# Performance work log

Hardware: AMD Instinct MI355X
Metric: run time of the kernel (lower is better)

Reference implementation:

```python
import jax, jax.numpy as jnp
import numpy as np

NUM_HEADS = 16
D_MODEL = 1024
D_K = D_MODEL // NUM_HEADS
B, S = 2, 2048


def setup_inputs() -> dict:
    key = jax.random.key(0)
    ks = jax.random.split(key, 10)
    q = jax.random.normal(ks[0], (B, S, D_MODEL), dtype=jnp.float32)
    k = jax.random.normal(ks[1], (B, S, D_MODEL), dtype=jnp.float32)
    v = jax.random.normal(ks[2], (B, S, D_MODEL), dtype=jnp.float32)
    # causal mask, 1 = keep, 0 = masked (masked_fill(mask==0, -1e9))
    mask = jnp.tril(jnp.ones((S, S), dtype=jnp.int32))[None, None, :, :]
    # Linear weights ~ N(0, 0.02); biases left at torch default-ish small uniform
    std = 0.02
    Wq = jax.random.normal(ks[3], (D_MODEL, D_MODEL), dtype=jnp.float32) * std
    Wk = jax.random.normal(ks[4], (D_MODEL, D_MODEL), dtype=jnp.float32) * std
    Wv = jax.random.normal(ks[5], (D_MODEL, D_MODEL), dtype=jnp.float32) * std
    bound = 1.0 / np.sqrt(D_MODEL)
    bq = jax.random.uniform(ks[6], (D_MODEL,), jnp.float32, -bound, bound)
    bk = jax.random.uniform(ks[7], (D_MODEL,), jnp.float32, -bound, bound)
    bv = jax.random.uniform(ks[8], (D_MODEL,), jnp.float32, -bound, bound)
    return {"q": q, "k": k, "v": v, "mask": mask,
            "Wq": Wq, "bq": bq, "Wk": Wk, "bk": bk, "Wv": Wv, "bv": bv}


def reference(q, k, v, mask, Wq, bq, Wk, bk, Wv, bv):
    # projections (torch Linear: x @ W.T + b), split heads -> [B, H, S, Dk]
    def proj(x, W, b):
        y = x @ W.T + b
        return y.reshape(B, S, NUM_HEADS, D_K).transpose(0, 2, 1, 3)

    qh, kh, vh = proj(q, Wq, bq), proj(k, Wk, bk), proj(v, Wv, bv)
    scores = jnp.einsum('bhqd,bhkd->bhqk', qh, kh) / jnp.sqrt(jnp.float32(D_K))
    scores = jnp.where(mask == 0, jnp.float32(-1e9), scores)
    p = jax.nn.softmax(scores, axis=-1)
    # dropout is identity in eval mode
    x = jnp.einsum('bhqk,bhkd->bhqd', p, vh)  # [B, H, S, Dk]
    return x.transpose(0, 2, 1, 3).reshape(B, S, D_MODEL)
```

## Files before the change

kernel.cpp:

```cpp
#include <hip/hip_runtime.h>

#define B_ 2
#define H_ 16
#define S_ 2048
#define DM 1024
#define DK 64
#define NX (4096 * 1024)

typedef unsigned short u16;
typedef __attribute__((ext_vector_type(8))) short bf16x8;
typedef __attribute__((ext_vector_type(8))) unsigned short u16x8;
typedef __attribute__((ext_vector_type(4))) unsigned short u16x4;
typedef __attribute__((ext_vector_type(2))) unsigned int u32x2;
typedef __attribute__((ext_vector_type(4))) unsigned int u32x4;
typedef __attribute__((ext_vector_type(4))) float f32x4;

__device__ inline u16 f2bf(float f) {
  union { float f; unsigned int u; } c; c.f = f;
  unsigned int u = c.u;
  u += 0x7fffu + ((u >> 16) & 1u);
  return (u16)(u >> 16);
}

__device__ inline void glds16(const u16* g, u16* l) {
  __builtin_amdgcn_global_load_lds(
      (const __attribute__((address_space(1))) unsigned int*)g,
      (__attribute__((address_space(3))) unsigned int*)l, 16, 0, 0);
}

__device__ inline unsigned cvtpk(float lo, float hi) {
  unsigned r;
  asm("v_cvt_pk_bf16_f32 %0, %1, %2" : "=v"(r) : "v"(lo), "v"(hi));
  return r;
}

__device__ inline void pub8(u16* d, float4 a, float4 b) {
  u32x4 r;
  r[0] = cvtpk(a.x, a.y); r[1] = cvtpk(a.z, a.w);
  r[2] = cvtpk(b.x, b.y); r[3] = cvtpk(b.z, b.w);
  *reinterpret_cast<u32x4*>(d) = r;
}

__global__ __launch_bounds__(256) void proj_kernel(
    const float* __restrict__ Xq, const float* __restrict__ Xk, const float* __restrict__ Xv,
    const float* __restrict__ Wq, const float* __restrict__ Wk, const float* __restrict__ Wv,
    const float* __restrict__ bq, const float* __restrict__ bk, const float* __restrict__ bv,
    u16* __restrict__ Qh, u16* __restrict__ Kh, u16* __restrict__ Vt)
{
  const int bid = blockIdx.x;
  const int xcd = bid & 7;
  const int tt  = bid >> 3;
  const int z   = tt >> 5;
  const int rr  = tt & 31;
  const int by  = xcd * 4 + (rr >> 3);
  const int bj  = rr & 7;

  const float* X    = (z == 0) ? Xq : (z == 1) ? Xk : Xv;
  const float* W    = (z == 0) ? Wq : (z == 1) ? Wk : Wv;
  const float* bias = (z == 0) ? bq : (z == 1) ? bk : bv;
  const float scale = (z == 0) ? 0.18033688f : 1.0f;

  __shared__ __align__(16) u16 Xs[128 * 32];
  __shared__ __align__(16) u16 Ws[128 * 32];

  const int tid = threadIdx.x;
  const int lane = tid & 63;
  const int w = tid >> 6;
  const int wy = w >> 1, wx = w & 1;
  const int m0 = by * 128;
  const int n0 = bj * 128;
  const int ml = lane & 15;
  const int qd = lane >> 4;

  const int r4 = lane >> 2;
  const int c8 = (lane & 3) * 8;
  const float* Xp0 = X + (size_t)(m0 + w * 16 + r4) * DM + c8;
  const float* Xp1 = X + (size_t)(m0 + (4 + w) * 16 + r4) * DM + c8;
  const float* Wp0 = W + (size_t)(n0 + w * 16 + r4) * DM + c8;
  const float* Wp1 = W + (size_t)(n0 + (4 + w) * 16 + r4) * DM + c8;
  u16* xd0 = &Xs[w * 512 + r4 * 32 + c8];
  u16* xd1 = &Xs[(4 + w) * 512 + r4 * 32 + c8];
  u16* wd0 = &Ws[w * 512 + r4 * 32 + c8];
  u16* wd1 = &Ws[(4 + w) * 512 + r4 * 32 + c8];

  f32x4 acc[4][4] = {};

  float4 xa0 = *(const float4*)(Xp0),     xb0 = *(const float4*)(Xp0 + 4);
  float4 xa1 = *(const float4*)(Xp1),     xb1 = *(const float4*)(Xp1 + 4);
  float4 wa0 = *(const float4*)(Wp0),     wb0 = *(const float4*)(Wp0 + 4);
  float4 wa1 = *(const float4*)(Wp1),     wb1 = *(const float4*)(Wp1 + 4);

  for (int kb = 0; kb < DM; kb += 32) {
    pub8(xd0, xa0, xb0);
    pub8(xd1, xa1, xb1);
    pub8(wd0, wa0, wb0);
    pub8(wd1, wa1, wb1);
    if (kb + 32 < DM) {
      const int kn = kb + 32;
      xa0 = *(const float4*)(Xp0 + kn); xb0 = *(const float4*)(Xp0 + kn + 4);
      xa1 = *(const float4*)(Xp1 + kn); xb1 = *(const float4*)(Xp1 + kn + 4);
      wa0 = *(const float4*)(Wp0 + kn); wb0 = *(const float4*)(Wp0 + kn + 4);
      wa1 = *(const float4*)(Wp1 + kn); wb1 = *(const float4*)(Wp1 + kn + 4);
    }
    asm volatile("s_waitcnt lgkmcnt(0)" ::: "memory");
    __builtin_amdgcn_s_barrier();
    asm volatile("" ::: "memory");

    bf16x8 a[4], bfr[4];
    #pragma unroll
    for (int i = 0; i < 4; ++i)
      a[i] = *reinterpret_cast<const bf16x8*>(&Xs[(wy * 64 + i * 16 + ml) * 32 + qd * 8]);
    #pragma unroll
    for (int j = 0; j < 4; ++j)
      bfr[j] = *reinterpret_cast<const bf16x8*>(&Ws[(wx * 64 + j * 16 + ml) * 32 + qd * 8]);
    #pragma unroll
    for (int i = 0; i < 4; ++i)
      #pragma unroll
      for (int j = 0; j < 4; ++j)
        acc[i][j] = __builtin_amdgcn_mfma_f32_16x16x32_bf16(a[i], bfr[j], acc[i][j], 0, 0, 0);

    asm volatile("" ::: "memory");
    __builtin_amdgcn_s_barrier();
    asm volatile("" ::: "memory");
  }

  if (z == 2) {
    #pragma unroll
    for (int j = 0; j < 4; ++j) {
      const int n = n0 + wx * 64 + j * 16 + ml;
      const float badd = bias[n];
      const int h = n >> 6, d = n & 63;
      #pragma unroll
      for (int i = 0; i < 4; ++i) {
        const int mb = m0 + wy * 64 + i * 16 + qd * 4;
        const int bi = mb >> 11, s0 = mb & 2047;
        u16x4 pk4;
        #pragma unroll
        for (int r = 0; r < 4; ++r) pk4[r] = f2bf(acc[i][j][r] + badd);
        *reinterpret_cast<u16x4*>(&Vt[((size_t)(bi * H_ + h) * DK + d) * S_ + s0]) = pk4;
      }
    }
  } else {
    u16* out = (z == 0) ? Qh : Kh;
    #pragma unroll
    for (int j = 0; j < 4; ++j) {
      const int n = n0 + wx * 64 + j * 16 + ml;
      const float badd = bias[n];
      const int h = n >> 6, d = n & 63;
      #pragma unroll
      for (int i = 0; i < 4; ++i) {
        #pragma unroll
        for (int r = 0; r < 4; ++r) {
          const int m = m0 + wy * 64 + i * 16 + qd * 4 + r;
          const int bi = m >> 11, s = m & 2047;
          out[((bi * H_ + h) * S_ + s) * DK + d] = f2bf((acc[i][j][r] + badd) * scale);
        }
      }
    }
  }
}

__global__ __launch_bounds__(256) void attn_kernel(
    const u16* __restrict__ Qh, const u16* __restrict__ Kh,
    const u16* __restrict__ Vt, float* __restrict__ out)
{
  __shared__ __align__(16) u16 Ks[2][64 * 64];
  __shared__ __align__(16) u16 Vs[2][64 * 64];
  __shared__ __align__(16) u16 Ps[4][2][16 * 64];

  const int tid  = threadIdx.x;
  const int lane = tid & 63;
  const int w    = tid >> 6;

  const int fid = blockIdx.x;
  const int bh  = (fid & 7) * 4 + ((fid >> 3) & 3);
  const int qt  = 15 - (fid >> 5);
  const int b   = bh >> 4, h = bh & 15;
  const int ml  = lane & 15, qd = lane >> 4;
  const int m7  = ml & 7;
  const int u0  = qd ^ m7;
  const int qh  = qd >> 1, ql = qd & 1;
  const int R0  = qt * 128;
  const int nt  = 2 * qt + 2;

  bf16x8 qa[2][2];
  #pragma unroll
  for (int g = 0; g < 2; ++g)
    #pragma unroll
    for (int ch = 0; ch < 2; ++ch)
      qa[g][ch] = *reinterpret_cast<const bf16x8*>(
          &Qh[((size_t)bh * S_ + R0 + w * 32 + g * 16 + ml) * DK + ch * 32 + qd * 8]);
  asm volatile("s_waitcnt vmcnt(0)" ::: "memory");

  const u16* kb0 = Kh + (size_t)bh * S_ * DK;
  const u16* vb0 = Vt + (size_t)bh * DK * S_;
  const int r0 = tid >> 3, r1 = r0 + 32;
  const int cs = (tid & 7) ^ (r0 & 7);
  const u16* sK0 = kb0 + r0 * DK + cs * 8;
  const u16* sK1 = kb0 + r1 * DK + cs * 8;
  const u16* sV0 = vb0 + (size_t)r0 * S_ + cs * 8;
  const u16* sV1 = vb0 + (size_t)r1 * S_ + cs * 8;

  f32x4 oacc[2][4] = {};
  float lsum[2] = {0.f, 0.f};

  glds16(sK0, &Ks[0][tid * 8]);
  glds16(sK1, &Ks[0][2048 + tid * 8]);
  glds16(sV0, &Vs[0][tid * 8]);
  glds16(sV1, &Vs[0][2048 + tid * 8]);
  sK0 += 4096; sK1 += 4096; sV0 += 64; sV1 += 64;

  int cur = 0;
  for (int t = 0; t < nt; ++t) {
    if (t + 1 < nt) {
      glds16(sK0, &Ks[cur ^ 1][tid * 8]);
      glds16(sK1, &Ks[cur ^ 1][2048 + tid * 8]);
      glds16(sV0, &Vs[cur ^ 1][tid * 8]);
      glds16(sV1, &Vs[cur ^ 1][2048 + tid * 8]);
      sK0 += 4096; sK1 += 4096; sV0 += 64; sV1 += 64;
      asm volatile("s_waitcnt vmcnt(4)" ::: "memory");
    } else {
      asm volatile("s_waitcnt vmcnt(0)" ::: "memory");
    }
    __builtin_amdgcn_s_barrier();
    asm volatile("" ::: "memory");

    const u16* Kb = Ks[cur];
    const u16* Vb = Vs[cur];

    const int d16_0 = (R0 + w * 32 - t * 64) >> 4;
    const int d16_1 = d16_0 + 1;
    const int jtop  = (d16_1 < 3) ? d16_1 : 3;

    if (jtop >= 0) {
      #pragma unroll
      for (int j = 0; j < 4; ++j) {
        if (j > jtop) break;
        const int rk = (j * 16 + ml) * 64;
        const bf16x8 k0 = *reinterpret_cast<const bf16x8*>(&Kb[rk + u0 * 8]);
        const bf16x8 k1 = *reinterpret_cast<const bf16x8*>(&Kb[rk + (u0 ^ 4) * 8]);
        #pragma unroll
        for (int g = 0; g < 2; ++g) {
          const int d16g = d16_0 + g;
          if (j > d16g) continue;
          f32x4 zz = {};
          zz = __builtin_amdgcn_mfma_f32_16x16x32_bf16(k0, qa[g][0], zz, 0, 0, 0);
          zz = __builtin_amdgcn_mfma_f32_16x16x32_bf16(k1, qa[g][1], zz, 0, 0, 0);
          if (j == d16g) {
            #pragma unroll
            for (int r = 0; r < 4; ++r)
              if (qd * 4 + r > ml) zz[r] = -1e30f;
          }
          const float e0 = __builtin_amdgcn_exp2f(zz[0]);
          const float e1 = __builtin_amdgcn_exp2f(zz[1]);
          const float e2 = __builtin_amdgcn_exp2f(zz[2]);
          const float e3 = __builtin_amdgcn_exp2f(zz[3]);
          lsum[g] += (e0 + e1) + (e2 + e3);
          u32x2 pk;
          pk[0] = cvtpk(e0, e1);
          pk[1] = cvtpk(e2, e3);
          *reinterpret_cast<u32x2*>(
              &Ps[w][g][ml * 64 + (((2 * j + qh) ^ m7) * 8) + ql * 4]) = pk;
        }
      }
      #pragma unroll
      for (int g = 0; g < 2; ++g) {
        const int d16g = d16_0 + g;
        if (d16g == 0 || d16g == 2) {
          const int jz = d16g + 1;
          *reinterpret_cast<u32x2*>(
              &Ps[w][g][ml * 64 + (((2 * jz + qh) ^ m7) * 8) + ql * 4]) = (u32x2){0, 0};
        }
      }
      #pragma unroll
      for (int c = 0; c < 2; ++c) {
        const bool use0 = d16_0 >= 2 * c;
        const bool use1 = d16_1 >= 2 * c;
        if (!(use0 | use1)) continue;
        bf16x8 vb[4];
        #pragma unroll
        for (int dj = 0; dj < 4; ++dj)
          vb[dj] = *reinterpret_cast<const bf16x8*>(
              &Vb[(dj * 16 + ml) * 64 + (u0 ^ (c << 2)) * 8]);
        if (use0) {
          const bf16x8 pa = *reinterpret_cast<const bf16x8*>(
              &Ps[w][0][ml * 64 + (u0 ^ (c << 2)) * 8]);
          #pragma unroll
          for (int dj = 0; dj < 4; ++dj)
            oacc[0][dj] = __builtin_amdgcn_mfma_f32_16x16x32_bf16(pa, vb[dj], oacc[0][dj], 0, 0, 0);
        }
        if (use1) {
          const bf16x8 pa = *reinterpret_cast<const bf16x8*>(
              &Ps[w][1][ml * 64 + (u0 ^ (c << 2)) * 8]);
          #pragma unroll
          for (int dj = 0; dj < 4; ++dj)
            oacc[1][dj] = __builtin_amdgcn_mfma_f32_16x16x32_bf16(pa, vb[dj], oacc[1][dj], 0, 0, 0);
        }
      }
    }

    asm volatile("" ::: "memory");
    __builtin_amdgcn_s_barrier();
    asm volatile("" ::: "memory");
    cur ^= 1;
  }

  #pragma unroll
  for (int g = 0; g < 2; ++g) {
    float lg = lsum[g];
    lg += __shfl_xor(lg, 16, 64);
    lg += __shfl_xor(lg, 32, 64);
    #pragma unroll
    for (int r = 0; r < 4; ++r) {
      const float inv = 1.0f / __shfl(lg, qd * 4 + r, 64);
      const int srow = R0 + w * 32 + g * 16 + qd * 4 + r;
      float* op = &out[(size_t)(b * S_ + srow) * DM + h * DK + ml];
      #pragma unroll
      for (int dj = 0; dj < 4; ++dj)
        op[dj * 16] = oacc[g][dj][r] * inv;
    }
  }
}

extern "C" void kernel_launch(void* const* d_in, const int* in_sizes, int n_in,
                              void* d_out, int out_size, void* d_ws, size_t ws_size,
                              hipStream_t stream) {
  const float* q  = (const float*)d_in[0];
  const float* k  = (const float*)d_in[1];
  const float* v  = (const float*)d_in[2];
  const float* Wq = (const float*)d_in[4];
  const float* bq = (const float*)d_in[5];
  const float* Wk = (const float*)d_in[6];
  const float* bk = (const float*)d_in[7];
  const float* Wv = (const float*)d_in[8];
  const float* bv = (const float*)d_in[9];

  u16* Qh = (u16*)d_ws;
  u16* Kh = Qh + NX;
  u16* Vt = Kh + NX;

  proj_kernel<<<dim3(768), 256, 0, stream>>>(
      q, k, v, Wq, Wk, Wv, bq, bk, bv, Qh, Kh, Vt);
  attn_kernel<<<dim3(512), 256, 0, stream>>>(
      Qh, Kh, Vt, (float*)d_out);
}
```

Measured before the change: 216.2 us.

## Double-buffer projection GEMM LDS tiles with padded rows and deeper prefetch

The QKV projection GEMM now uses two LDS buffers per operand, with the row stride padded from 32 to 40 elements to reduce bank conflicts. It keeps two K-steps of global loads in flight in registers. Each half-iteration stages into its own buffer, which removes one barrier per K-step. This raises register and LDS usage, which may lower occupancy.

```diff
diff --git a/kernel.cpp b/kernel.cpp
--- a/kernel.cpp
+++ b/kernel.cpp
@@ -6,6 +6,7 @@
 #define DM 1024
 #define DK 64
 #define NX (4096 * 1024)
+#define LW 40
 
 typedef unsigned short u16;
 typedef __attribute__((ext_vector_type(8))) short bf16x8;
@@ -60,8 +61,8 @@
   const float* bias = (z == 0) ? bq : (z == 1) ? bk : bv;
   const float scale = (z == 0) ? 0.18033688f : 1.0f;
 
-  __shared__ __align__(16) u16 Xs[128 * 32];
-  __shared__ __align__(16) u16 Ws[128 * 32];
+  __shared__ __align__(16) u16 Xs[2][128 * LW];
+  __shared__ __align__(16) u16 Ws[2][128 * LW];
 
   const int tid = threadIdx.x;
   const int lane = tid & 63;
@@ -74,54 +75,83 @@
 
   const int r4 = lane >> 2;
   const int c8 = (lane & 3) * 8;
-  const float* Xp0 = X + (size_t)(m0 + w * 16 + r4) * DM + c8;
-  const float* Xp1 = X + (size_t)(m0 + (4 + w) * 16 + r4) * DM + c8;
-  const float* Wp0 = W + (size_t)(n0 + w * 16 + r4) * DM + c8;
-  const float* Wp1 = W + (size_t)(n0 + (4 + w) * 16 + r4) * DM + c8;
-  u16* xd0 = &Xs[w * 512 + r4 * 32 + c8];
-  u16* xd1 = &Xs[(4 + w) * 512 + r4 * 32 + c8];
-  u16* wd0 = &Ws[w * 512 + r4 * 32 + c8];
-  u16* wd1 = &Ws[(4 + w) * 512 + r4 * 32 + c8];
+  const int row0 = w * 16 + r4, row1 = (4 + w) * 16 + r4;
+  const float* Xp0 = X + (size_t)(m0 + row0) * DM + c8;
+  const float* Xp1 = X + (size_t)(m0 + row1) * DM + c8;
+  const float* Wp0 = W + (size_t)(n0 + row0) * DM + c8;
+  const float* Wp1 = W + (size_t)(n0 + row1) * DM + c8;
+  const int xo0 = row0 * LW + c8, xo1 = row1 * LW + c8;
 
   f32x4 acc[4][4] = {};
 
-  float4 xa0 = *(const float4*)(Xp0),     xb0 = *(const float4*)(Xp0 + 4);
-  float4 xa1 = *(const float4*)(Xp1),     xb1 = *(const float4*)(Xp1 + 4);
-  float4 wa0 = *(const float4*)(Wp0),     wb0 = *(const float4*)(Wp0 + 4);
-  float4 wa1 = *(const float4*)(Wp1),     wb1 = *(const float4*)(Wp1 + 4);
-
-  for (int kb = 0; kb < DM; kb += 32) {
-    pub8(xd0, xa0, xb0);
-    pub8(xd1, xa1, xb1);
-    pub8(wd0, wa0, wb0);
-    pub8(wd1, wa1, wb1);
-    if (kb + 32 < DM) {
-      const int kn = kb + 32;
-      xa0 = *(const float4*)(Xp0 + kn); xb0 = *(const float4*)(Xp0 + kn + 4);
-      xa1 = *(const float4*)(Xp1 + kn); xb1 = *(const float4*)(Xp1 + kn + 4);
-      wa0 = *(const float4*)(Wp0 + kn); wb0 = *(const float4*)(Wp0 + kn + 4);
-      wa1 = *(const float4*)(Wp1 + kn); wb1 = *(const float4*)(Wp1 + kn + 4);
+  float4 Axa0 = *(const float4*)(Xp0),      Axb0 = *(const float4*)(Xp0 + 4);
+  float4 Axa1 = *(const float4*)(Xp1),      Axb1 = *(const float4*)(Xp1 + 4);
+  float4 Awa0 = *(const float4*)(Wp0),      Awb0 = *(const float4*)(Wp0 + 4);
+  float4 Awa1 = *(const float4*)(Wp1),      Awb1 = *(const float4*)(Wp1 + 4);
+  float4 Bxa0 = *(const float4*)(Xp0 + 32), Bxb0 = *(const float4*)(Xp0 + 36);
+  float4 Bxa1 = *(const float4*)(Xp1 + 32), Bxb1 = *(const float4*)(Xp1 + 36);
+  float4 Bwa0 = *(const float4*)(Wp0 + 32), Bwb0 = *(const float4*)(Wp0 + 36);
+  float4 Bwa1 = *(const float4*)(Wp1 + 32), Bwb1 = *(const float4*)(Wp1 + 36);
+
+  #pragma unroll 1
+  for (int kb = 0; kb < DM; kb += 64) {
+    pub8(&Xs[0][xo0], Axa0, Axb0);
+    pub8(&Xs[0][xo1], Axa1, Axb1);
+    pub8(&Ws[0][xo0], Awa0, Awb0);
+    pub8(&Ws[0][xo1], Awa1, Awb1);
+    if (kb + 64 < DM) {
+      const int kn = kb + 64;
+      Axa0 = *(const float4*)(Xp0 + kn); Axb0 = *(const float4*)(Xp0 + kn + 4);
+      Axa1 = *(const float4*)(Xp1 + kn); Axb1 = *(const float4*)(Xp1 + kn + 4);
+      Awa0 = *(const float4*)(Wp0 + kn); Awb0 = *(const float4*)(Wp0 + kn + 4);
+      Awa1 = *(const float4*)(Wp1 + kn); Awb1 = *(const float4*)(Wp1 + kn + 4);
     }
     asm volatile("s_waitcnt lgkmcnt(0)" ::: "memory");
     __builtin_amdgcn_s_barrier();
     asm volatile("" ::: "memory");
-
-    bf16x8 a[4], bfr[4];
-    #pragma unroll
-    for (int i = 0; i < 4; ++i)
-      a[i] = *reinterpret_cast<const bf16x8*>(&Xs[(wy * 64 + i * 16 + ml) * 32 + qd * 8]);
-    #pragma unroll
-    for (int j = 0; j < 4; ++j)
-      bfr[j] = *reinterpret_cast<const bf16x8*>(&Ws[(wx * 64 + j * 16 + ml) * 32 + qd * 8]);
-    #pragma unroll
-    for (int i = 0; i < 4; ++i)
+    {
+      bf16x8 a[4], bfr[4];
+      #pragma unroll
+      for (int i = 0; i < 4; ++i)
+        a[i] = *reinterpret_cast<const bf16x8*>(&Xs[0][(wy * 64 + i * 16 + ml) * LW + qd * 8]);
       #pragma unroll
       for (int j = 0; j < 4; ++j)
-        acc[i][j] = __builtin_amdgcn_mfma_f32_16x16x32_bf16(a[i], bfr[j], acc[i][j], 0, 0, 0);
-
-    asm volatile("" ::: "memory");
+        bfr[j] = *reinterpret_cast<const bf16x8*>(&Ws[0][(wx * 64 + j * 16 + ml) * LW + qd * 8]);
+      #pragma unroll
+      for (int i = 0; i < 4; ++i)
+        #pragma unroll
+        for (int j = 0; j < 4; ++j)
+          acc[i][j] = __builtin_amdgcn_mfma_f32_16x16x32_bf16(a[i], bfr[j], acc[i][j], 0, 0, 0);
+    }
+
+    pub8(&Xs[1][xo0], Bxa0, Bxb0);
+    pub8(&Xs[1][xo1], Bxa1, Bxb1);
+    pub8(&Ws[1][xo0], Bwa0, Bwb0);
+    pub8(&Ws[1][xo1], Bwa1, Bwb1);
+    if (kb + 96 < DM) {
+      const int kn = kb + 96;
+      Bxa0 = *(const float4*)(Xp0 + kn); Bxb0 = *(const float4*)(Xp0 + kn + 4);
+      Bxa1 = *(const float4*)(Xp1 + kn); Bxb1 = *(const float4*)(Xp1 + kn + 4);
+      Bwa0 = *(const float4*)(Wp0 + kn); Bwb0 = *(const float4*)(Wp0 + kn + 4);
+      Bwa1 = *(const float4*)(Wp1 + kn); Bwb1 = *(const float4*)(Wp1 + kn + 4);
+    }
+    asm volatile("s_waitcnt lgkmcnt(0)" ::: "memory");
     __builtin_amdgcn_s_barrier();
     asm volatile("" ::: "memory");
+    {
+      bf16x8 a[4], bfr[4];
+      #pragma unroll
+      for (int i = 0; i < 4; ++i)
+        a[i] = *reinterpret_cast<const bf16x8*>(&Xs[1][(wy * 64 + i * 16 + ml) * LW + qd * 8]);
+      #pragma unroll
+      for (int j = 0; j < 4; ++j)
+        bfr[j] = *reinterpret_cast<const bf16x8*>(&Ws[1][(wx * 64 + j * 16 + ml) * LW + qd * 8]);
+      #pragma unroll
+      for (int i = 0; i < 4; ++i)
+        #pragma unroll
+        for (int j = 0; j < 4; ++j)
+          acc[i][j] = __builtin_amdgcn_mfma_f32_16x16x32_bf16(a[i], bfr[j], acc[i][j], 0, 0, 0);
+    }
   }
 
   if (z == 2) {
```

Measured after the change: 214.1 us. Within noise of the previous version (-1.0%).
